# Kernel tuning notes

Measured on AMD Instinct MI355X. Metric: run time of the kernel, lower is better.

## Reference

```python
import jax, jax.numpy as jnp
from jax import lax
import numpy as np

B, C, L = 64, 32, 1549
HID = 256          # LSTM hidden per direction
NH, DK = 8, 64     # n_heads, d_k ; NH*DK = 2*HID = 512
D2 = 2 * HID


def setup_inputs() -> dict:
    key = jax.random.key(0)
    ks = jax.random.split(key, 32)
    r = lambda i, shape: jax.random.normal(ks[i], shape, jnp.float32) * 0.05
    inp = {"x": jax.random.normal(ks[0], (B, C, L), jnp.float32)}
    inp["conv_w"] = r(1, (C, C, 16))
    inp["conv_b"] = r(2, (C,))
    inp["bn_gamma"] = 1.0 + r(3, (C,))
    inp["bn_beta"] = r(4, (C,))
    inp["bn_mean"] = r(5, (C,))
    inp["bn_var"] = jax.random.uniform(ks[6], (C,), jnp.float32, 0.5, 1.5)
    names = [("W_ih0f", (4*HID, C)), ("W_hh0f", (4*HID, HID)), ("b0f", (4*HID,)),
             ("W_ih0b", (4*HID, C)), ("W_hh0b", (4*HID, HID)), ("b0b", (4*HID,)),
             ("W_ih1f", (4*HID, D2)), ("W_hh1f", (4*HID, HID)), ("b1f", (4*HID,)),
             ("W_ih1b", (4*HID, D2)), ("W_hh1b", (4*HID, HID)), ("b1b", (4*HID,)),
             ("Wq", (D2, D2)), ("bq", (D2,)), ("Wk", (D2, D2)), ("bk", (D2,)),
             ("Wv", (D2, D2)), ("bv", (D2,)), ("ln_g", (D2,)), ("ln_b", (D2,)),
             ("fc_w", (1, D2)), ("fc_b", (1,))]
    for j, (n, s) in enumerate(names):
        inp[n] = r(7 + j, s)
    inp["ln_g"] = 1.0 + inp["ln_g"]
    return inp


def _lstm_dir(xg, W_hh, reverse):
    # xg: [B,S,4H] precomputed input-to-gate projections (+biases); PyTorch gate order i,f,g,o
    if reverse:
        xg = xg[:, ::-1]
    Bq = xg.shape[0]
    H = W_hh.shape[1]
    def step(carry, g_t):
        h, c = carry
        g = g_t + h @ W_hh.T
        i, f, gg, o = jnp.split(g, 4, axis=-1)
        c = jax.nn.sigmoid(f) * c + jax.nn.sigmoid(i) * jnp.tanh(gg)
        h = jax.nn.sigmoid(o) * jnp.tanh(c)
        return (h, c), h
    init = (jnp.zeros((Bq, H), xg.dtype), jnp.zeros((Bq, H), xg.dtype))
    _, hs = lax.scan(step, init, jnp.swapaxes(xg, 0, 1))
    hs = jnp.swapaxes(hs, 0, 1)
    return hs[:, ::-1] if reverse else hs


def _bilstm(x, Wif, Whf, bf, Wib, Whb, bb):
    hf = _lstm_dir(jnp.einsum('bsd,gd->bsg', x, Wif) + bf, Whf, False)
    hb = _lstm_dir(jnp.einsum('bsd,gd->bsg', x, Wib) + bb, Whb, True)
    return jnp.concatenate([hf, hb], axis=-1)


def _forward(x, conv_w, conv_b, bn_gamma, bn_beta, bn_mean, bn_var,
             W_ih0f, W_hh0f, b0f, W_ih0b, W_hh0b, b0b,
             W_ih1f, W_hh1f, b1f, W_ih1b, W_hh1b, b1b,
             Wq, bq, Wk, bk, Wv, bv, ln_g, ln_b, fc_w, fc_b):
    # conv1d (k=16, pad=1) + BatchNorm (eval) + relu + maxpool(k=3, stride=3)
    h = lax.conv_general_dilated(x, conv_w, (1,), [(1, 1)],
                                 dimension_numbers=('NCH', 'OIH', 'NCH')) + conv_b[None, :, None]
    h = (h - bn_mean[None, :, None]) * jax.lax.rsqrt(bn_var[None, :, None] + 1e-5) \
        * bn_gamma[None, :, None] + bn_beta[None, :, None]
    h = jax.nn.relu(h)
    h = lax.reduce_window(h, -jnp.inf, lax.max, (1, 1, 3), (1, 1, 3), 'VALID')
    h = jnp.transpose(h, (0, 2, 1))            # [B, S, C]
    # 2-layer bidirectional LSTM (eval: inter-layer dropout inactive)
    out = _bilstm(h, W_ih0f, W_hh0f, b0f, W_ih0b, W_hh0b, b0b)
    out = _bilstm(out, W_ih1f, W_hh1f, b1f, W_ih1b, W_hh1b, b1b)   # [B, S, 512]
    Bq, S, _ = out.shape
    q = (out @ Wq.T + bq).reshape(Bq, S, NH, DK).transpose(0, 2, 1, 3)
    k = (out @ Wk.T + bk).reshape(Bq, S, NH, DK).transpose(0, 2, 1, 3)
    v = (out @ Wv.T + bv).reshape(Bq, S, NH, DK).transpose(0, 2, 1, 3)
    attn = jnp.einsum('bhsd,bhtd->bhst', q, k) / np.sqrt(DK)
    # NOTE: original uses nn.LogSoftmax(dim=1) -> log-softmax over the HEAD axis
    la = jax.nn.log_softmax(attn, axis=1)
    ctx = jnp.einsum('bhst,bhtd->bhsd', la, v)
    ctx = jnp.transpose(ctx, (0, 2, 1, 3)).reshape(Bq, S, D2)
    r = out + ctx
    mu = jnp.mean(r, axis=-1, keepdims=True)
    var = jnp.mean((r - mu) ** 2, axis=-1, keepdims=True)
    r = (r - mu) * jax.lax.rsqrt(var + 1e-5) * ln_g + ln_b
    pooled = jnp.mean(r, axis=1)               # len_reduction='mean'
    return pooled @ fc_w.T + fc_b              # [B, 1]


def reference(x, conv_w, conv_b, bn_gamma, bn_beta, bn_mean, bn_var,
              W_ih0f, W_hh0f, b0f, W_ih0b, W_hh0b, b0b,
              W_ih1f, W_hh1f, b1f, W_ih1b, W_hh1b, b1b,
              Wq, bq, Wk, bk, Wv, bv, ln_g, ln_b, fc_w, fc_b):
    return _forward(x, conv_w, conv_b, bn_gamma, bn_beta, bn_mean, bn_var,
                    W_ih0f, W_hh0f, b0f, W_ih0b, W_hh0b, b0b,
                    W_ih1f, W_hh1f, b1f, W_ih1b, W_hh1b, b1b,
                    Wq, bq, Wk, bk, Wv, bv, ln_g, ln_b, fc_w, fc_b)
```

## Files before the change

### kernel.cpp

```cpp
#include <hip/hip_runtime.h>
#include <hip/hip_bf16.h>
#include <math.h>

#define L_IN 1549
#define S_OUT 512

typedef __hip_bfloat16 bf16;
typedef __attribute__((ext_vector_type(8))) short bfrag;
typedef __attribute__((ext_vector_type(4))) float f32x4;

__device__ __forceinline__ float bfbits2f(unsigned short u) {
    union { unsigned int i; float f; } x;
    x.i = ((unsigned int)u) << 16;
    return x.f;
}
__device__ __forceinline__ unsigned short f2bfbits(float f) {
    union { float f; unsigned int i; } x; x.f = f;
    unsigned int lsb = (x.i >> 16) & 1;
    return (unsigned short)((x.i + 0x7fff + lsb) >> 16);
}

__device__ __forceinline__ float fast_sig(float x) {
    float e = __builtin_amdgcn_exp2f(-1.442695041f * x);
    return __builtin_amdgcn_rcpf(1.f + e);
}
__device__ __forceinline__ float fast_tanh(float x) {
    float e = __builtin_amdgcn_exp2f(2.885390082f * x);
    return 1.f - 2.f * __builtin_amdgcn_rcpf(1.f + e);
}

#if __has_builtin(__builtin_amdgcn_fdot2_f32_bf16)
typedef __attribute__((ext_vector_type(2))) __bf16 v2bf;
__device__ __forceinline__ float dot2bf(unsigned int w, unsigned int h, float c) {
    union { unsigned int u; v2bf v; } a, b;
    a.u = w; b.u = h;
    return __builtin_amdgcn_fdot2_f32_bf16(a.v, b.v, c, false);
}
#else
__device__ __forceinline__ float dot2bf(unsigned int w, unsigned int h, float c) {
    union { unsigned int i; float f; } w0, w1, h0, h1;
    w0.i = w << 16; w1.i = w & 0xffff0000u;
    h0.i = h << 16; h1.i = h & 0xffff0000u;
    return c + w0.f * h0.f + w1.f * h1.f;
}
#endif

__global__ __launch_bounds__(256) void conv_bn_pool(
    const float* __restrict__ x, const float* __restrict__ w,
    const float* __restrict__ cb, const float* __restrict__ gamma,
    const float* __restrict__ beta, const float* __restrict__ mean,
    const float* __restrict__ var, bf16* __restrict__ h0)
{
    int b  = blockIdx.y;
    int sg = blockIdx.x;
    __shared__ float xs[32][40];
    int tid = threadIdx.x;
    int base = sg * 24;
    for (int i = tid; i < 32 * 40; i += 256) {
        int ci = i / 40, dl = i % 40;
        int l = base - 1 + dl;
        xs[ci][dl] = (l >= 0 && l < L_IN) ? x[(size_t)(b * 32 + ci) * L_IN + l] : 0.f;
    }
    __syncthreads();
    int c = tid & 31, sl = tid >> 5;
    float scale = gamma[c] * rsqrtf(var[c] + 1e-5f);
    float shift = beta[c] - mean[c] * scale;
    float bias = cb[c];
    float acc0 = bias, acc1 = bias, acc2 = bias;
    int off0 = 3 * sl;
    for (int ci = 0; ci < 32; ++ci) {
        const float* wrp = w + (size_t)(c * 32 + ci) * 16;
        float4 w0 = *(const float4*)(wrp);
        float4 w1 = *(const float4*)(wrp + 4);
        float4 w2 = *(const float4*)(wrp + 8);
        float4 w3 = *(const float4*)(wrp + 12);
        float wk[16] = {w0.x, w0.y, w0.z, w0.w, w1.x, w1.y, w1.z, w1.w,
                        w2.x, w2.y, w2.z, w2.w, w3.x, w3.y, w3.z, w3.w};
        const float* xr = &xs[ci][off0];
        #pragma unroll
        for (int kk = 0; kk < 16; ++kk) {
            float xv0 = xr[kk];
            float xv1 = xr[kk + 1];
            float xv2 = xr[kk + 2];
            acc0 += xv0 * wk[kk];
            acc1 += xv1 * wk[kk];
            acc2 += xv2 * wk[kk];
        }
    }
    float y0 = fmaxf(acc0 * scale + shift, 0.f);
    float y1 = fmaxf(acc1 * scale + shift, 0.f);
    float y2 = fmaxf(acc2 * scale + shift, 0.f);
    float best = fmaxf(fmaxf(y0, y1), y2);
    int s = sg * 8 + sl;
    h0[((size_t)b * S_OUT + s) * 32 + c] = __float2bfloat16(best);
}

__global__ void pack_lstm4(
    const float* __restrict__ W0, const float* __restrict__ W1,
    const float* __restrict__ W2, const float* __restrict__ W3,
    unsigned int* __restrict__ outbase)
{
    int set = blockIdx.y;
    const float* W = (set == 0) ? W0 : (set == 1) ? W1 : (set == 2) ? W2 : W3;
    unsigned int* out = outbase + (size_t)set * 131072;
    int i = blockIdx.x * 256 + threadIdx.x;
    int kp, t, col;
    if (i < 102400) {
        kp = i >> 10; col = (i >> 9) & 1; t = i & 511;
    } else if (i < 116736) {
        int j = i - 102400;
        kp = 100 + (j >> 10); t = (j & 1023) >> 1; col = j & 1;
    } else {
        int j = i - 116736;
        kp = 114 + (j >> 10); t = (j & 1023) >> 1; col = j & 1;
    }
    int g = 2 * t + col;
    unsigned int lo = f2bfbits(W[(size_t)g * 256 + 2 * kp]);
    unsigned int hi = f2bfbits(W[(size_t)g * 256 + 2 * kp + 1]);
    out[i] = lo | (hi << 16);
}

__global__ __launch_bounds__(256) void pack_b7(
    const float* __restrict__ A0, const float* __restrict__ A1,
    const float* __restrict__ A2, const float* __restrict__ A3,
    const float* __restrict__ A4, const float* __restrict__ A5,
    const float* __restrict__ A6, unsigned short* __restrict__ out)
{
    int i = blockIdx.x * 256 + threadIdx.x;
    const float* src; int j;
    if      (i <   32768) { src = A0; j = i; }
    else if (i <   65536) { src = A1; j = i - 32768; }
    else if (i <  589824) { src = A2; j = i - 65536; }
    else if (i < 1114112) { src = A3; j = i - 589824; }
    else if (i < 1376256) { src = A4; j = i - 1114112; }
    else if (i < 1638400) { src = A5; j = i - 1376256; }
    else if (i < 1900544) { src = A6; j = i - 1638400; }
    else return;
    out[i] = f2bfbits(src[j]);
}

#define LDA 40
__global__ __launch_bounds__(256) void gemm_mfma(
    const bf16* __restrict__ A,
    const bf16* __restrict__ Bm0, const bf16* __restrict__ Bm1, const bf16* __restrict__ Bm2,
    const float* __restrict__ bs0, const float* __restrict__ bs1, const float* __restrict__ bs2,
    bf16* __restrict__ Cm0, bf16* __restrict__ Cm1, bf16* __restrict__ Cm2,
    int M, int N, int K)
{
    int nbn = N >> 7;
    int nbm = M >> 7;
    int lid = blockIdx.x;
    int xcd = lid & 7;
    int slot = lid >> 3;
    int bn = slot % nbn;
    int pair = xcd + 8 * (slot / nbn);
    int bm = pair % nbm;
    int z  = pair / nbm;

    const bf16* B = (z == 0) ? Bm0 : ((z == 1) ? Bm1 : Bm2);
    const float* bias = (z == 0) ? bs0 : ((z == 1) ? bs1 : bs2);
    bf16* C = (z == 0) ? Cm0 : ((z == 1) ? Cm1 : Cm2);

    __shared__ bf16 As[128 * LDA];
    __shared__ bf16 Bs[128 * LDA];

    int tid = threadIdx.x;
    int lane = tid & 63;
    int wave = tid >> 6;
    int wm = (wave >> 1) * 64;
    int wn = (wave & 1) * 64;

    int sr = tid >> 2;
    int sc = (tid & 3) * 8;
    const bf16* Ag = A + (size_t)(bm * 128 + sr) * K + sc;
    const bf16* Bg = B + (size_t)(bn * 128 + sr) * K + sc;

    int fm = lane & 15;
    int fk = (lane >> 4) * 8;

    f32x4 acc[4][4];
    #pragma unroll
    for (int i = 0; i < 4; ++i)
        #pragma unroll
        for (int j = 0; j < 4; ++j) acc[i][j] = (f32x4)(0.f);

    for (int k0 = 0; k0 < K; k0 += 32) {
        float4 a0 = *(const float4*)(Ag + k0);
        float4 a1 = *(const float4*)(Ag + (size_t)64 * K + k0);
        float4 b0 = *(const float4*)(Bg + k0);
        float4 b1 = *(const float4*)(Bg + (size_t)64 * K + k0);
        __syncthreads();
        *(float4*)(As + sr * LDA + sc)        = a0;
        *(float4*)(As + (sr + 64) * LDA + sc) = a1;
        *(float4*)(Bs + sr * LDA + sc)        = b0;
        *(float4*)(Bs + (sr + 64) * LDA + sc) = b1;
        __syncthreads();

        bfrag af[4], bfr[4];
        #pragma unroll
        for (int i = 0; i < 4; ++i)
            af[i] = *(const bfrag*)(As + (wm + i * 16 + fm) * LDA + fk);
        #pragma unroll
        for (int j = 0; j < 4; ++j)
            bfr[j] = *(const bfrag*)(Bs + (wn + j * 16 + fm) * LDA + fk);
        #pragma unroll
        for (int i = 0; i < 4; ++i)
            #pragma unroll
            for (int j = 0; j < 4; ++j)
                acc[i][j] = __builtin_amdgcn_mfma_f32_16x16x32_bf16(
                    af[i], bfr[j], acc[i][j], 0, 0, 0);
    }

    int rbase = (lane >> 4) * 4;
    #pragma unroll
    for (int j = 0; j < 4; ++j) {
        int n = bn * 128 + wn + j * 16 + (lane & 15);
        float bv = bias[n];
        #pragma unroll
        for (int i = 0; i < 4; ++i) {
            #pragma unroll
            for (int r = 0; r < 4; ++r) {
                int m = bm * 128 + wm + i * 16 + rbase + r;
                C[(size_t)m * N + n] = __float2bfloat16(acc[i][j][r] + bv);
            }
        }
    }
}

__global__ __launch_bounds__(512, 2) void lstm_reg(
    const bf16* __restrict__ xg_f, const bf16* __restrict__ xg_b,
    const unsigned int* __restrict__ Wl, bf16* __restrict__ out)
{
    int u = blockIdx.x;
    int b = u & 63, dir = u >> 6;
    const unsigned int* W = Wl + (size_t)dir * 131072;
    const bf16* xg = dir ? xg_b : xg_f;
    int t = threadIdx.x;

    __shared__ unsigned int lw[14336];
    __shared__ __align__(16) unsigned int hsb[2][128];
    __shared__ float gsh[1024];

    unsigned int wr[200];
    #pragma unroll
    for (int j = 0; j < 200; ++j) wr[j] = W[j * 512 + t];
    for (int i = t; i < 14336; i += 512) lw[i] = W[102400 + i];
    if (t < 128) { hsb[0][t] = 0u; }
    float cst = 0.f;
    __syncthreads();

    const unsigned int* Wst = W + 116736;
    int par = 0;
    unsigned short hb = 0;
    size_t oaddr = 0;
    bool have_out = false;

    for (int step = 0; step < 512; ++step) {
        int ts = dir ? (511 - step) : step;

        uint2 sw[14];
        #pragma unroll
        for (int s = 0; s < 14; ++s)
            sw[s] = *(const uint2*)(Wst + s * 1024 + 2 * t);
        unsigned int xv =
            *(const unsigned int*)(xg + ((size_t)b * 512 + ts) * 1024 + 2 * t);

        const unsigned int* hs = hsb[par];
        float a0 = 0.f, a1 = 0.f;
        #pragma unroll
        for (int q = 0; q < 32; ++q) {
            uint4 hv = *(const uint4*)&hs[q * 4];
            #pragma unroll
            for (int r = 0; r < 4; ++r) {
                int kp = q * 4 + r;
                unsigned int h2 = (&hv.x)[r];
                if (kp < 100) {
                    a0 = dot2bf(wr[kp * 2], h2, a0);
                    a1 = dot2bf(wr[kp * 2 + 1], h2, a1);
                } else if (kp < 114) {
                    uint2 wv = *(const uint2*)&lw[(kp - 100) * 1024 + 2 * t];
                    a0 = dot2bf(wv.x, h2, a0);
                    a1 = dot2bf(wv.y, h2, a1);
                } else {
                    a0 = dot2bf(sw[kp - 114].x, h2, a0);
                    a1 = dot2bf(sw[kp - 114].y, h2, a1);
                }
            }
        }
        a0 += bfbits2f((unsigned short)(xv & 0xffff));
        a1 += bfbits2f((unsigned short)(xv >> 16));

        *(float2*)&gsh[2 * t] = make_float2(a0, a1);
        __syncthreads();

        if (t < 256) {
            float gi = gsh[t], gf = gsh[256 + t], gg = gsh[512 + t], go = gsh[768 + t];
            float si = fast_sig(gi);
            float sf = fast_sig(gf);
            float so = fast_sig(go);
            cst = sf * cst + si * fast_tanh(gg);
            float h = so * fast_tanh(cst);
            hb = f2bfbits(h);
            ((unsigned short*)hsb[par ^ 1])[t] = hb;
            oaddr = ((size_t)b * 512 + ts) * 512 + dir * 256 + t;
            have_out = true;
        }
        __syncthreads();
        if (have_out) {
            *(unsigned short*)(out + oaddr) = hb;
            have_out = false;
        }
        par ^= 1;
    }
}

__global__ __launch_bounds__(256) void vt_transpose(
    const bf16* __restrict__ v, bf16* __restrict__ vt)
{
    __shared__ unsigned short tile[64 * 73];
    int b = blockIdx.z;
    int s0 = blockIdx.x * 64, n0 = blockIdx.y * 64;
    int tid = threadIdx.x;
    #pragma unroll
    for (int u = 0; u < 2; ++u) {
        int idx = tid + u * 256;
        int si = idx >> 3, nj = (idx & 7) << 3;
        bfrag val = *(const bfrag*)(v + ((size_t)(b * 512 + s0 + si)) * 512 + n0 + nj);
        #pragma unroll
        for (int jj = 0; jj < 8; ++jj)
            tile[(nj + jj) * 73 + si] = ((unsigned short*)&val)[jj];
    }
    __syncthreads();
    #pragma unroll
    for (int u = 0; u < 2; ++u) {
        int idx = tid + u * 256;
        int ni = idx >> 3, sj = (idx & 7) << 3;
        unsigned short outv[8];
        #pragma unroll
        for (int jj = 0; jj < 8; ++jj)
            outv[jj] = tile[ni * 73 + sj + jj];
        *(float4*)(vt + (size_t)b * 262144 + (size_t)(n0 + ni) * 512 + s0 + sj) =
            *(float4*)outv;
    }
}

__global__ __launch_bounds__(256, 2) void attention_mfma(
    const bf16* __restrict__ q, const bf16* __restrict__ k,
    const bf16* __restrict__ vt, bf16* r)
{
    int n_ = blockIdx.x;
    int xcd = n_ & 7;
    int slot = n_ >> 3;
    int b = xcd + ((slot >> 4) << 3);
    int s0 = (slot & 15) * 32;
    int tid = threadIdx.x;
    int wave = tid >> 6;
    int sw = wave & 1, dh = wave >> 1;
    int lane = tid & 63;
    int L15 = lane & 15, quad = lane >> 4;

    const bf16* qrow = q + ((size_t)(b * 512 + s0 + sw * 16 + L15)) * 512;
    bfrag qf[8][2];
    #pragma unroll
    for (int h = 0; h < 8; ++h) {
        qf[h][0] = *(const bfrag*)(qrow + h * 64 + quad * 8);
        qf[h][1] = *(const bfrag*)(qrow + h * 64 + 32 + quad * 8);
    }

    f32x4 ctxa[8][2];
    #pragma unroll
    for (int h = 0; h < 8; ++h) {
        ctxa[h][0] = (f32x4)(0.f);
        ctxa[h][1] = (f32x4)(0.f);
    }

    int tperm = ((L15 >> 2) << 3) + (L15 & 3);
    const bf16* kbase = k + (size_t)(b * 512) * 512;
    const bf16* vbase = vt + (size_t)b * 262144;

    for (int tc = 0; tc < 512; tc += 32) {
        f32x4 sa[8][2];
        #pragma unroll
        for (int h = 0; h < 8; ++h) {
            #pragma unroll
            for (int tile = 0; tile < 2; ++tile) {
                const bf16* krow = kbase
                    + (size_t)(tc + tile * 4 + tperm) * 512 + h * 64 + quad * 8;
                bfrag a0 = *(const bfrag*)(krow);
                bfrag a1 = *(const bfrag*)(krow + 32);
                f32x4 acc = __builtin_amdgcn_mfma_f32_16x16x32_bf16(
                    a0, qf[h][0], (f32x4)(0.f), 0, 0, 0);
                acc = __builtin_amdgcn_mfma_f32_16x16x32_bf16(
                    a1, qf[h][1], acc, 0, 0, 0);
                sa[h][tile] = acc;
            }
        }
        bfrag pf[8];
        #pragma unroll
        for (int tile = 0; tile < 2; ++tile) {
            #pragma unroll
            for (int rr = 0; rr < 4; ++rr) {
                float sc[8];
                float m = -1e30f;
                #pragma unroll
                for (int h = 0; h < 8; ++h) {
                    sc[h] = sa[h][tile][rr] * 0.125f;
                    m = fmaxf(m, sc[h]);
                }
                float sum = 0.f;
                #pragma unroll
                for (int h = 0; h < 8; ++h)
                    sum += __builtin_amdgcn_exp2f((sc[h] - m) * 1.442695041f);
                float lse = m + 0.6931471806f * __builtin_amdgcn_logf(sum);
                #pragma unroll
                for (int h = 0; h < 8; ++h)
                    ((unsigned short*)&pf[h])[tile * 4 + rr] = f2bfbits(sc[h] - lse);
            }
        }
        #pragma unroll
        for (int h = 0; h < 8; ++h) {
            #pragma unroll
            for (int dt = 0; dt < 2; ++dt) {
                int n = h * 64 + dh * 32 + dt * 16 + L15;
                bfrag vf = *(const bfrag*)(vbase + (size_t)n * 512 + tc + quad * 8);
                ctxa[h][dt] = __builtin_amdgcn_mfma_f32_16x16x32_bf16(
                    pf[h], vf, ctxa[h][dt], 0, 0, 0);
            }
        }
    }
    #pragma unroll
    for (int h = 0; h < 8; ++h) {
        #pragma unroll
        for (int dt = 0; dt < 2; ++dt) {
            int n = h * 64 + dh * 32 + dt * 16 + L15;
            #pragma unroll
            for (int rr = 0; rr < 4; ++rr) {
                size_t addr =
                    ((size_t)(b * 512 + s0 + sw * 16 + quad * 4 + rr)) * 512 + n;
                float o = __bfloat162float(r[addr]);
                r[addr] = __float2bfloat16(o + ctxa[h][dt][rr]);
            }
        }
    }
}

__global__ __launch_bounds__(512) void ln_pool_fc(
    const bf16* __restrict__ r, const float* __restrict__ g, const float* __restrict__ bt,
    const float* __restrict__ fcw, const float* __restrict__ fcb, float* __restrict__ out)
{
    int b = blockIdx.y;
    int s = blockIdx.x * 8 + (threadIdx.x >> 6);
    int lane = threadIdx.x & 63;
    int n0 = lane * 8;

    float gf[8];
    float btf = 0.f;
    #pragma unroll
    for (int j = 0; j < 8; ++j) {
        float fw = fcw[n0 + j];
        gf[j] = g[n0 + j] * fw;
        btf += bt[n0 + j] * fw;
    }

    bfrag rv = *(const bfrag*)(r + ((size_t)(b * 512 + s)) * 512 + n0);
    float v[8];
    float s1 = 0.f, s2 = 0.f;
    #pragma unroll
    for (int j = 0; j < 8; ++j) {
        v[j] = bfbits2f(((const unsigned short*)&rv)[j]);
        s1 += v[j];
        s2 += v[j] * v[j];
    }
    #pragma unroll
    for (int off = 32; off > 0; off >>= 1) {
        s1 += __shfl_xor(s1, off);
        s2 += __shfl_xor(s2, off);
    }
    float mu = s1 * (1.f / 512.f);
    float var = s2 * (1.f / 512.f) - mu * mu;
    float rs = rsqrtf(var + 1e-5f);

    float d = 0.f;
    #pragma unroll
    for (int j = 0; j < 8; ++j) d += (v[j] - mu) * gf[j];
    #pragma unroll
    for (int off = 32; off > 0; off >>= 1) {
        d += __shfl_down(d, off);
        btf += __shfl_down(btf, off);
    }
    if (lane == 0) {
        float val = d * rs * (1.f / 512.f);
        if (s == 0) val += btf + fcb[0];
        atomicAdd(out + b, val);
    }
}

extern "C" void kernel_launch(void* const* d_in, const int* in_sizes, int n_in,
                              void* d_out, int out_size, void* d_ws, size_t ws_size,
                              hipStream_t stream)
{
    (void)in_sizes; (void)n_in; (void)ws_size;
    const float* x      = (const float*)d_in[0];
    const float* conv_w = (const float*)d_in[1];
    const float* conv_b = (const float*)d_in[2];
    const float* bn_g   = (const float*)d_in[3];
    const float* bn_b   = (const float*)d_in[4];
    const float* bn_m   = (const float*)d_in[5];
    const float* bn_v   = (const float*)d_in[6];
    const float* W_ih0f = (const float*)d_in[7];
    const float* W_hh0f = (const float*)d_in[8];
    const float* b0f    = (const float*)d_in[9];
    const float* W_ih0b = (const float*)d_in[10];
    const float* W_hh0b = (const float*)d_in[11];
    const float* b0b    = (const float*)d_in[12];
    const float* W_ih1f = (const float*)d_in[13];
    const float* W_hh1f = (const float*)d_in[14];
    const float* b1f    = (const float*)d_in[15];
    const float* W_ih1b = (const float*)d_in[16];
    const float* W_hh1b = (const float*)d_in[17];
    const float* b1b    = (const float*)d_in[18];
    const float* Wq = (const float*)d_in[19];
    const float* bq = (const float*)d_in[20];
    const float* Wk = (const float*)d_in[21];
    const float* bk = (const float*)d_in[22];
    const float* Wv = (const float*)d_in[23];
    const float* bv = (const float*)d_in[24];
    const float* ln_g = (const float*)d_in[25];
    const float* ln_b = (const float*)d_in[26];
    const float* fc_w = (const float*)d_in[27];
    const float* fc_b = (const float*)d_in[28];
    float* out = (float*)d_out;

    char* ws = (char*)d_ws;
    bf16* xgf  = (bf16*)ws;
    bf16* xgb  = xgf + 33554432;
    bf16* out0 = (bf16*)(ws + 134217728);
    bf16* out1 = (bf16*)(ws + 167772160);
    bf16* h0   = (bf16*)(ws + 201326592);
    unsigned int* wl0 = (unsigned int*)(ws + 203423744);
    unsigned int* wl1 = wl0 + 262144;
    bf16* wpk  = (bf16*)(ws + 205520896);
    bf16* qb = xgf;
    bf16* kb = xgf + 16777216;
    bf16* vb = xgb;
    bf16* vtb = out0;

    hipMemsetAsync(d_out, 0, (size_t)out_size * sizeof(float), stream);

    pack_lstm4<<<dim3(512, 4), 256, 0, stream>>>(
        W_hh0f, W_hh0b, W_hh1f, W_hh1b, wl0);

    pack_b7<<<7424, 256, 0, stream>>>(
        W_ih0f, W_ih0b, W_ih1f, W_ih1b, Wq, Wk, Wv, (unsigned short*)wpk);

    conv_bn_pool<<<dim3(64, 64), 256, 0, stream>>>(
        x, conv_w, conv_b, bn_g, bn_b, bn_m, bn_v, h0);

    gemm_mfma<<<4096, 256, 0, stream>>>(
        h0, wpk, wpk + 32768, nullptr, b0f, b0b, nullptr, xgf, xgb, nullptr,
        32768, 1024, 32);

    lstm_reg<<<128, 512, 0, stream>>>(xgf, xgb, wl0, out0);

    gemm_mfma<<<4096, 256, 0, stream>>>(
        out0, wpk + 65536, wpk + 589824, nullptr, b1f, b1b, nullptr,
        xgf, xgb, nullptr, 32768, 1024, 512);

    lstm_reg<<<128, 512, 0, stream>>>(xgf, xgb, wl1, out1);

    gemm_mfma<<<3072, 256, 0, stream>>>(
        out1, wpk + 1114112, wpk + 1376256, wpk + 1638400, bq, bk, bv,
        qb, kb, vb, 32768, 512, 512);

    vt_transpose<<<dim3(8, 8, 64), 256, 0, stream>>>(vb, vtb);

    attention_mfma<<<1024, 256, 0, stream>>>(qb, kb, vtb, out1);

    ln_pool_fc<<<dim3(64, 64), 512, 0, stream>>>(out1, ln_g, ln_b, fc_w, fc_b, out);
}
```

Before: 2.734 ms.

## Split LSTM recurrent matvec K across thread halves with 4-gate vectorized weights

Each LSTM thread now computes partial sums for 4 consecutive gates over half of the hidden dimension, instead of 2 gates over all of it. The two halves are combined through a doubled shared-memory gate buffer. The weight packing is rearranged so register, LDS and streamed weights can all be loaded as uint4. The aim is more independent accumulators for ILP and fewer, wider loads per step. The cost is an extra shared-memory read and add per gate in the activation phase.

```diff
diff --git a/kernel.cpp b/kernel.cpp
--- a/kernel.cpp
+++ b/kernel.cpp
@@ -104,17 +104,19 @@
     const float* W = (set == 0) ? W0 : (set == 1) ? W1 : (set == 2) ? W2 : W3;
     unsigned int* out = outbase + (size_t)set * 131072;
     int i = blockIdx.x * 256 + threadIdx.x;
-    int kp, t, col;
+    int kpl, j;
     if (i < 102400) {
-        kp = i >> 10; col = (i >> 9) & 1; t = i & 511;
+        kpl = i >> 11; j = i & 2047;
     } else if (i < 116736) {
-        int j = i - 102400;
-        kp = 100 + (j >> 10); t = (j & 1023) >> 1; col = j & 1;
+        int m = i - 102400;
+        kpl = 50 + (m >> 11); j = m & 2047;
     } else {
-        int j = i - 116736;
-        kp = 114 + (j >> 10); t = (j & 1023) >> 1; col = j & 1;
-    }
-    int g = 2 * t + col;
+        int m = i - 116736;
+        kpl = 57 + (m >> 11); j = m & 2047;
+    }
+    int t = j >> 2, gi = j & 3;
+    int g = 4 * (t & 255) + gi;
+    int kp = (t >> 8) * 64 + kpl;
     unsigned int lo = f2bfbits(W[(size_t)g * 256 + 2 * kp]);
     unsigned int hi = f2bfbits(W[(size_t)g * 256 + 2 * kp + 1]);
     out[i] = lo | (hi << 16);
@@ -239,11 +241,12 @@
 
     __shared__ unsigned int lw[14336];
     __shared__ __align__(16) unsigned int hsb[2][128];
-    __shared__ float gsh[1024];
+    __shared__ __align__(16) float gsh[2][1024];
 
     unsigned int wr[200];
     #pragma unroll
-    for (int j = 0; j < 200; ++j) wr[j] = W[j * 512 + t];
+    for (int j = 0; j < 50; ++j)
+        *(uint4*)&wr[j * 4] = *(const uint4*)&W[j * 2048 + 4 * t];
     for (int i = t; i < 14336; i += 512) lw[i] = W[102400 + i];
     if (t < 128) { hsb[0][t] = 0u; }
     float cst = 0.f;
@@ -251,50 +254,69 @@
 
     const unsigned int* Wst = W + 116736;
     int par = 0;
+    int khalf = t >> 8;
+    int gq = t & 255;
+    const unsigned int* lwp = lw + 4 * t;
     unsigned short hb = 0;
     size_t oaddr = 0;
-    bool have_out = false;
 
     for (int step = 0; step < 512; ++step) {
         int ts = dir ? (511 - step) : step;
 
-        uint2 sw[14];
-        #pragma unroll
-        for (int s = 0; s < 14; ++s)
-            sw[s] = *(const uint2*)(Wst + s * 1024 + 2 * t);
-        unsigned int xv =
-            *(const unsigned int*)(xg + ((size_t)b * 512 + ts) * 1024 + 2 * t);
-
-        const unsigned int* hs = hsb[par];
-        float a0 = 0.f, a1 = 0.f;
-        #pragma unroll
-        for (int q = 0; q < 32; ++q) {
+        uint4 sv[7];
+        #pragma unroll
+        for (int s = 0; s < 7; ++s)
+            sv[s] = *(const uint4*)&Wst[s * 2048 + 4 * t];
+        uint2 xv = make_uint2(0u, 0u);
+        if (khalf == 0)
+            xv = *(const uint2*)(xg + ((size_t)b * 512 + ts) * 1024 + 4 * t);
+
+        const unsigned int* hs = hsb[par] + khalf * 64;
+        float a0 = 0.f, a1 = 0.f, a2 = 0.f, a3 = 0.f;
+        #pragma unroll
+        for (int q = 0; q < 16; ++q) {
             uint4 hv = *(const uint4*)&hs[q * 4];
             #pragma unroll
             for (int r = 0; r < 4; ++r) {
-                int kp = q * 4 + r;
+                int kpl = q * 4 + r;
                 unsigned int h2 = (&hv.x)[r];
-                if (kp < 100) {
-                    a0 = dot2bf(wr[kp * 2], h2, a0);
-                    a1 = dot2bf(wr[kp * 2 + 1], h2, a1);
-                } else if (kp < 114) {
-                    uint2 wv = *(const uint2*)&lw[(kp - 100) * 1024 + 2 * t];
+                if (kpl < 50) {
+                    const unsigned int* w4 = &wr[kpl * 4];
+                    a0 = dot2bf(w4[0], h2, a0);
+                    a1 = dot2bf(w4[1], h2, a1);
+                    a2 = dot2bf(w4[2], h2, a2);
+                    a3 = dot2bf(w4[3], h2, a3);
+                } else if (kpl < 57) {
+                    uint4 wv = *(const uint4*)&lwp[(kpl - 50) * 2048];
                     a0 = dot2bf(wv.x, h2, a0);
                     a1 = dot2bf(wv.y, h2, a1);
+                    a2 = dot2bf(wv.z, h2, a2);
+                    a3 = dot2bf(wv.w, h2, a3);
                 } else {
-                    a0 = dot2bf(sw[kp - 114].x, h2, a0);
-                    a1 = dot2bf(sw[kp - 114].y, h2, a1);
+                    uint4 wv = sv[kpl - 57];
+                    a0 = dot2bf(wv.x, h2, a0);
+                    a1 = dot2bf(wv.y, h2, a1);
+                    a2 = dot2bf(wv.z, h2, a2);
+                    a3 = dot2bf(wv.w, h2, a3);
                 }
             }
         }
-        a0 += bfbits2f((unsigned short)(xv & 0xffff));
-        a1 += bfbits2f((unsigned short)(xv >> 16));
-
-        *(float2*)&gsh[2 * t] = make_float2(a0, a1);
+        if (khalf == 0) {
+            a0 += bfbits2f((unsigned short)(xv.x & 0xffff));
+            a1 += bfbits2f((unsigned short)(xv.x >> 16));
+            a2 += bfbits2f((unsigned short)(xv.y & 0xffff));
+            a3 += bfbits2f((unsigned short)(xv.y >> 16));
+        }
+
+        *(float4*)&gsh[khalf][4 * gq] = make_float4(a0, a1, a2, a3);
         __syncthreads();
 
-        if (t < 256) {
-            float gi = gsh[t], gf = gsh[256 + t], gg = gsh[512 + t], go = gsh[768 + t];
+        bool act = (t < 256);
+        if (act) {
+            float gi = gsh[0][t]       + gsh[1][t];
+            float gf = gsh[0][256 + t] + gsh[1][256 + t];
+            float gg = gsh[0][512 + t] + gsh[1][512 + t];
+            float go = gsh[0][768 + t] + gsh[1][768 + t];
             float si = fast_sig(gi);
             float sf = fast_sig(gf);
             float so = fast_sig(go);
@@ -303,13 +325,9 @@
             hb = f2bfbits(h);
             ((unsigned short*)hsb[par ^ 1])[t] = hb;
             oaddr = ((size_t)b * 512 + ts) * 512 + dir * 256 + t;
-            have_out = true;
         }
         __syncthreads();
-        if (have_out) {
-            *(unsigned short*)(out + oaddr) = hb;
-            have_out = false;
-        }
+        if (act) *(unsigned short*)(out + oaddr) = hb;
         par ^= 1;
     }
 }
```

Result: no change. 2.719 ms (-0.5%).

## Permute LSTM gate layout so gate nonlinearity uses lane shuffles instead of LDS barrier

Applied to the files above, without the earlier changes.

Reorders the packed recurrent weights and the input-gate GEMM output columns so each thread pair holds all four gates (i,g on even lane, f,o on odd) for one hidden unit. The gate values are exchanged with __shfl_xor, which removes the shared-memory gate buffer and one __syncthreads per timestep in the serial LSTM loop. In exchange, only half the threads run the nonlinearity, and the GEMM epilogue writes scattered columns, which may hurt store coalescing.

```diff
diff --git a/kernel.cpp b/kernel.cpp
--- a/kernel.cpp
+++ b/kernel.cpp
@@ -114,7 +114,7 @@
         int j = i - 116736;
         kp = 114 + (j >> 10); t = (j & 1023) >> 1; col = j & 1;
     }
-    int g = 2 * t + col;
+    int g = ((t & 1) << 8) + (t >> 1) + (col << 9);
     unsigned int lo = f2bfbits(W[(size_t)g * 256 + 2 * kp]);
     unsigned int hi = f2bfbits(W[(size_t)g * 256 + 2 * kp + 1]);
     out[i] = lo | (hi << 16);
@@ -145,7 +145,7 @@
     const bf16* __restrict__ Bm0, const bf16* __restrict__ Bm1, const bf16* __restrict__ Bm2,
     const float* __restrict__ bs0, const float* __restrict__ bs1, const float* __restrict__ bs2,
     bf16* __restrict__ Cm0, bf16* __restrict__ Cm1, bf16* __restrict__ Cm2,
-    int M, int N, int K)
+    int M, int N, int K, int cperm)
 {
     int nbn = N >> 7;
     int nbm = M >> 7;
@@ -216,12 +216,13 @@
     for (int j = 0; j < 4; ++j) {
         int n = bn * 128 + wn + j * 16 + (lane & 15);
         float bv = bias[n];
+        int np = cperm ? (((n & 255) << 2) | (((n >> 8) & 1) << 1) | ((n >> 9) & 1)) : n;
         #pragma unroll
         for (int i = 0; i < 4; ++i) {
             #pragma unroll
             for (int r = 0; r < 4; ++r) {
                 int m = bm * 128 + wm + i * 16 + rbase + r;
-                C[(size_t)m * N + n] = __float2bfloat16(acc[i][j][r] + bv);
+                C[(size_t)m * N + np] = __float2bfloat16(acc[i][j][r] + bv);
             }
         }
     }
@@ -239,7 +240,6 @@
 
     __shared__ unsigned int lw[14336];
     __shared__ __align__(16) unsigned int hsb[2][128];
-    __shared__ float gsh[1024];
 
     unsigned int wr[200];
     #pragma unroll
@@ -253,7 +253,8 @@
     int par = 0;
     unsigned short hb = 0;
     size_t oaddr = 0;
-    bool have_out = false;
+    bool act = (t & 1) == 0;
+    int n = t >> 1;
 
     for (int step = 0; step < 512; ++step) {
         int ts = dir ? (511 - step) : step;
@@ -290,26 +291,20 @@
         a0 += bfbits2f((unsigned short)(xv & 0xffff));
         a1 += bfbits2f((unsigned short)(xv >> 16));
 
-        *(float2*)&gsh[2 * t] = make_float2(a0, a1);
-        __syncthreads();
-
-        if (t < 256) {
-            float gi = gsh[t], gf = gsh[256 + t], gg = gsh[512 + t], go = gsh[768 + t];
-            float si = fast_sig(gi);
-            float sf = fast_sig(gf);
-            float so = fast_sig(go);
-            cst = sf * cst + si * fast_tanh(gg);
+        float fb = __shfl_xor(a0, 1);
+        float ob = __shfl_xor(a1, 1);
+        if (act) {
+            float si = fast_sig(a0);
+            float sf = fast_sig(fb);
+            float so = fast_sig(ob);
+            cst = sf * cst + si * fast_tanh(a1);
             float h = so * fast_tanh(cst);
             hb = f2bfbits(h);
-            ((unsigned short*)hsb[par ^ 1])[t] = hb;
-            oaddr = ((size_t)b * 512 + ts) * 512 + dir * 256 + t;
-            have_out = true;
+            ((unsigned short*)hsb[par ^ 1])[n] = hb;
+            oaddr = ((size_t)b * 512 + ts) * 512 + dir * 256 + n;
         }
         __syncthreads();
-        if (have_out) {
-            *(unsigned short*)(out + oaddr) = hb;
-            have_out = false;
-        }
+        if (act) *(unsigned short*)(out + oaddr) = hb;
         par ^= 1;
     }
 }
@@ -558,19 +553,19 @@
 
     gemm_mfma<<<4096, 256, 0, stream>>>(
         h0, wpk, wpk + 32768, nullptr, b0f, b0b, nullptr, xgf, xgb, nullptr,
-        32768, 1024, 32);
+        32768, 1024, 32, 1);
 
     lstm_reg<<<128, 512, 0, stream>>>(xgf, xgb, wl0, out0);
 
     gemm_mfma<<<4096, 256, 0, stream>>>(
         out0, wpk + 65536, wpk + 589824, nullptr, b1f, b1b, nullptr,
-        xgf, xgb, nullptr, 32768, 1024, 512);
+        xgf, xgb, nullptr, 32768, 1024, 512, 1);
 
     lstm_reg<<<128, 512, 0, stream>>>(xgf, xgb, wl1, out1);
 
     gemm_mfma<<<3072, 256, 0, stream>>>(
         out1, wpk + 1114112, wpk + 1376256, wpk + 1638400, bq, bk, bv,
-        qb, kb, vb, 32768, 512, 512);
+        qb, kb, vb, 32768, 512, 512, 0);
 
     vt_transpose<<<dim3(8, 8, 64), 256, 0, stream>>>(vb, vtb);
 
```

Result: slower. 2.798 ms (+2.4%).
